# Kernel optimization log

Hardware: AMD Instinct MI355X
Metric: run time of the kernel (lower is better)

## Reference

```python
import jax, jax.numpy as jnp
import numpy as np
import math

A = 256            # n_agents == batch rows (epymarl stacks agents along batch)
B = A
OBS = 512          # obs_shape = (input_shape - n_actions) // 2
NA = 64            # n_actions
MSG = 2048         # messages_shape (divisible by A)
H = 1024           # hidden_dim
T = 3              # trajectory_length
TAU = OBS + NA
VD = MSG // A      # per-agent message dim


def setup_inputs() -> dict:
    key = jax.random.key(0)
    keys = iter(jax.random.split(key, 40))
    def lin(o, i):
        w = jax.random.normal(next(keys), (o, i), jnp.float32) * (i ** -0.5)
        return w, jnp.zeros((o,), jnp.float32)
    d = {}
    d["inputs"] = jax.random.normal(next(keys), (B, 2 * OBS + NA + MSG), jnp.float32)
    d["hidden_state"] = jax.random.normal(next(keys), (B, 3 * H), jnp.float32) * 0.1
    for name, o, i in [("pi_fc1", H, OBS + MSG), ("pi_fc2", NA, H),
                       ("fa_fc1", H, OBS), ("fa_fc2", (A - 1) * NA, H),
                       ("fo_fc1", H, NA * A + OBS), ("fo_fc2", OBS, H),
                       ("am_qs", H, MSG), ("am_ks", H, TAU), ("am_vs", VD, TAU)]:
        d[name + "_w"], d[name + "_b"] = lin(o, i)
    for name in ["pi_rnn", "fa_rnn", "fo_rnn"]:
        d[name + "_wih"], d[name + "_bih"] = lin(3 * H, H)
        d[name + "_whh"], d[name + "_bhh"] = lin(3 * H, H)
    return d


def _gru(x, h, wih, whh, bih, bhh):
    gi = x @ wih.T + bih
    gh = h @ whh.T + bhh
    ir, iz, i_n = jnp.split(gi, 3, -1)
    hr, hz, h_n = jnp.split(gh, 3, -1)
    r = jax.nn.sigmoid(ir + hr)
    z = jax.nn.sigmoid(iz + hz)
    n = jnp.tanh(i_n + r * h_n)
    return (1.0 - z) * n + z * h


def reference(inputs, hidden_state,
              pi_fc1_w, pi_fc1_b, pi_fc2_w, pi_fc2_b,
              pi_rnn_wih, pi_rnn_whh, pi_rnn_bih, pi_rnn_bhh,
              fa_fc1_w, fa_fc1_b, fa_fc2_w, fa_fc2_b,
              fa_rnn_wih, fa_rnn_whh, fa_rnn_bih, fa_rnn_bhh,
              fo_fc1_w, fo_fc1_b, fo_fc2_w, fo_fc2_b,
              fo_rnn_wih, fo_rnn_whh, fo_rnn_bih, fo_rnn_bhh,
              am_qs_w, am_qs_b, am_ks_w, am_ks_b, am_vs_w, am_vs_b):
    sg = jax.lax.stop_gradient
    lin = lambda x, w, b: x @ w.T + b
    h_fa = hidden_state[:, :H]
    h_fo = hidden_state[:, H:2 * H]
    h_pi0 = hidden_state[:, -H:]
    obs = inputs[:, :OBS]
    prev_obs = inputs[:, OBS:2 * OBS]
    prev_act = sg(inputs[:, 2 * OBS:2 * OBS + NA])   # .detach() in torch
    prev_msg = inputs[:, -MSG:]

    def pi(o, m, h):
        x = jax.nn.relu(lin(jnp.concatenate([o, m], -1), pi_fc1_w, pi_fc1_b))
        h2 = _gru(x, h, pi_rnn_wih, pi_rnn_whh, pi_rnn_bih, pi_rnn_bhh)
        return lin(h2, pi_fc2_w, pi_fc2_b), h2

    # ---- ImaginedTrajectory rollout (fixed small T, python loop is structural) ----
    o, a, h_pi = prev_obs, prev_act, h_pi0
    observations, actions = [o], [a]
    for _ in range(T - 1):
        x = jax.nn.relu(lin(o, fa_fc1_w, fa_fc1_b))
        h_fa = _gru(x, h_fa, fa_rnn_wih, fa_rnn_whh, fa_rnn_bih, fa_rnn_bhh)
        q = lin(h_fa, fa_fc2_w, fa_fc2_b)                       # [B,(A-1)*NA]
        qs = jax.nn.softmax(q.reshape(B, A - 1, NA), -1)
        # torch stack(qs_out).reshape(orig): scrambles (A-1,B) order, kept faithfully
        fa = jnp.transpose(qs, (1, 0, 2)).reshape(B, (A - 1) * NA)
        x2 = jax.nn.relu(lin(jnp.concatenate([fa, a, o], -1), fo_fc1_w, fo_fc1_b))
        h_fo = _gru(x2, h_fo, fo_rnn_wih, fo_rnn_whh, fo_rnn_bih, fo_rnn_bhh)
        nxt_o = lin(h_fo, fo_fc2_w, fo_fc2_b)
        nxt_a, h_pi = pi(sg(o), sg(prev_msg), sg(h_pi))         # forward_pi detaches inputs
        o, a = nxt_o, nxt_a
        observations.append(o)
        actions.append(a)
    taus = jnp.stack([jnp.concatenate([observations[t], actions[t]], -1)
                      for t in range(T)])                        # [T,B,TAU]

    # ---- AttentionMechanism: batched equivalent of the per-agent python loops ----
    # k rows are indexed j*n_agents + i with batch == n_agents, i.e. k[t, b] here.
    qv = lin(prev_msg, am_qs_w, am_qs_b)                         # [B,H]
    kk = jnp.einsum('tbi,hi->tbh', taus, am_ks_w) + am_ks_b      # [T,B,H]
    vv = jnp.einsum('tbi,vi->tbv', taus, am_vs_w) + am_vs_b      # [T,B,VD]
    alpha = jax.nn.softmax(jnp.einsum('bh,tbh->bt', qv, kk) / math.sqrt(H), -1)
    new_message = jnp.einsum('bt,tbv->bv', alpha, vv)            # [B,VD]

    # cat([msg]*A, 0).reshape(B,-1): each agent receives all agents' messages
    pi_msg = jnp.tile(new_message, (A, 1)).reshape(B, -1)        # [B,MSG]
    action, h_pi_f = pi(obs, pi_msg, h_pi0)                      # uses ORIGINAL h_pi slice
    h_out = jnp.concatenate([h_fa, h_fo, h_pi_f], -1)            # [B,3H]
    q_out = jnp.concatenate([new_message, action], -1)           # [B,VD+NA]
    return q_out, h_out
```

## Files before the change

### kernel.cpp

```cpp
#include <hip/hip_runtime.h>
#include <hip/hip_bf16.h>
#include <math.h>

#define OBS 512
#define MSG 2048
#define TAU 576
#define TAUP 640
#define QN 16320
#define X2W 16896
#define INW 3136
#define PIW 2560

typedef short short8v __attribute__((ext_vector_type(8)));
typedef float f32x4 __attribute__((ext_vector_type(4)));

__device__ inline unsigned bfbits(float x) {
  __hip_bfloat16 h = __float2bfloat16(x);
  return (unsigned)*reinterpret_cast<unsigned short*>(&h);
}

__device__ inline void gload16(const void* g, void* l) {
  __builtin_amdgcn_global_load_lds((__attribute__((address_space(1))) void*)(g),
                                   (__attribute__((address_space(3))) void*)(l), 16, 0, 0);
}

struct MMSet {
  const __hip_bfloat16* A;
  const __hip_bfloat16* W;
  const float* bias;
  float* C;
  __hip_bfloat16* Cb;
  int lda, ldw, ldc, ldcb;
};

template<int ACT, bool ATOMIC, bool DUAL>
__global__ __launch_bounds__(512)
void k_mm(MMSet s0, MMSet s1, int Nlim, int kSteps)
{
  __shared__ __hip_bfloat16 As[2][256 * 64];
  __shared__ __hip_bfloat16 Bs[2][64 * 64];
  const MMSet S = (DUAL && blockIdx.z) ? s1 : s0;
  const int tid = threadIdx.x;
  const int lane = tid & 63;
  const int wid = tid >> 6;
  const int m0 = blockIdx.y * 256;
  const int n0 = blockIdx.x * 64;
  const size_t k0 = ATOMIC ? (size_t)blockIdx.z * kSteps * 64 : 0;

  const __hip_bfloat16* Ab = S.A + (size_t)m0 * S.lda + k0;
  const __hip_bfloat16* Bb = S.W + (size_t)n0 * S.ldw + k0;

  int arow[4], acol[4], adst[4];
#pragma unroll
  for (int r = 0; r < 4; ++r) {
    int chunk = r * 512 + tid;
    arow[r] = chunk >> 3;
    acol[r] = ((chunk & 7) ^ (arow[r] & 7)) * 8;
    adst[r] = chunk * 8;
  }
  const int brow = tid >> 3;
  const int bcol = ((tid & 7) ^ (brow & 7)) * 8;
  const int bdst = tid * 8;

  const int wr = wid >> 1, wc = wid & 1;
  const int fr = lane & 15, q = lane >> 4;
  const int xm = fr & 7;

  f32x4 acc[4][2] = {};

  auto stage = [&](int buf, int kt) {
#pragma unroll
    for (int r = 0; r < 4; ++r)
      gload16(Ab + (size_t)arow[r] * S.lda + kt + acol[r], &As[buf][adst[r]]);
    gload16(Bb + (size_t)brow * S.ldw + kt + bcol, &Bs[buf][bdst]);
  };

  stage(0, 0);
  __syncthreads();

  for (int t = 0; t < kSteps; ++t) {
    if (t + 1 < kSteps) stage((t + 1) & 1, (t + 1) * 64);
    const __hip_bfloat16* Ac = As[t & 1];
    const __hip_bfloat16* Bc = Bs[t & 1];
#pragma unroll
    for (int ks = 0; ks < 2; ++ks) {
      const int cc = ks * 4 + q;
      const int co = ((cc ^ xm) << 3);
      short8v a0 = *(const short8v*)&Ac[(wr * 64 +  0 + fr) * 64 + co];
      short8v a1 = *(const short8v*)&Ac[(wr * 64 + 16 + fr) * 64 + co];
      short8v a2 = *(const short8v*)&Ac[(wr * 64 + 32 + fr) * 64 + co];
      short8v a3 = *(const short8v*)&Ac[(wr * 64 + 48 + fr) * 64 + co];
      short8v b0 = *(const short8v*)&Bc[(wc * 32 +  0 + fr) * 64 + co];
      short8v b1 = *(const short8v*)&Bc[(wc * 32 + 16 + fr) * 64 + co];
      acc[0][0] = __builtin_amdgcn_mfma_f32_16x16x32_bf16(a0, b0, acc[0][0], 0, 0, 0);
      acc[0][1] = __builtin_amdgcn_mfma_f32_16x16x32_bf16(a0, b1, acc[0][1], 0, 0, 0);
      acc[1][0] = __builtin_amdgcn_mfma_f32_16x16x32_bf16(a1, b0, acc[1][0], 0, 0, 0);
      acc[1][1] = __builtin_amdgcn_mfma_f32_16x16x32_bf16(a1, b1, acc[1][1], 0, 0, 0);
      acc[2][0] = __builtin_amdgcn_mfma_f32_16x16x32_bf16(a2, b0, acc[2][0], 0, 0, 0);
      acc[2][1] = __builtin_amdgcn_mfma_f32_16x16x32_bf16(a2, b1, acc[2][1], 0, 0, 0);
      acc[3][0] = __builtin_amdgcn_mfma_f32_16x16x32_bf16(a3, b0, acc[3][0], 0, 0, 0);
      acc[3][1] = __builtin_amdgcn_mfma_f32_16x16x32_bf16(a3, b1, acc[3][1], 0, 0, 0);
    }
    __syncthreads();
  }

#pragma unroll
  for (int i = 0; i < 4; ++i) {
    const int mb = m0 + wr * 64 + i * 16 + q * 4;
#pragma unroll
    for (int j = 0; j < 2; ++j) {
      const int n = n0 + wc * 32 + j * 16 + fr;
      if (n >= Nlim) continue;
      if (ATOMIC) {
#pragma unroll
        for (int v = 0; v < 4; ++v)
          atomicAdd(&S.C[(size_t)(mb + v) * S.ldc + n], acc[i][j][v]);
      } else {
        const float bb = S.bias[n];
#pragma unroll
        for (int v = 0; v < 4; ++v) {
          float val = acc[i][j][v] + bb;
          if (ACT) val = fmaxf(val, 0.f);
          if (S.C)  S.C[(size_t)(mb + v) * S.ldc + n] = val;
          if (S.Cb) S.Cb[(size_t)(mb + v) * S.ldcb + n] = __float2bfloat16(val);
        }
      }
    }
  }
}

struct CvtTable {
  const float* src[15];
  __hip_bfloat16* dst[15];
  long nchunk[15];
  int srcld[15], N[15], Kdst[15], Kval[15];
  int cumBlk[16];
};

__global__ __launch_bounds__(256)
void k_cvt_all(CvtTable T)
{
  const int bx = blockIdx.x;
  int sg = 0;
#pragma unroll
  for (int i = 1; i < 15; ++i) sg += (bx >= T.cumBlk[i]) ? 1 : 0;
  const float* src = T.src[0]; __hip_bfloat16* dst = T.dst[0];
  long nchunk = T.nchunk[0];
  int srcld = T.srcld[0], N = T.N[0], Kd = T.Kdst[0], Kv = T.Kval[0], b0 = T.cumBlk[0];
#pragma unroll
  for (int i = 1; i < 15; ++i)
    if (sg == i) { src = T.src[i]; dst = T.dst[i]; nchunk = T.nchunk[i];
                   srcld = T.srcld[i]; N = T.N[i]; Kd = T.Kdst[i]; Kv = T.Kval[i]; b0 = T.cumBlk[i]; }
  long chunk = (long)(bx - b0) * 256 + threadIdx.x;
  if (chunk >= nchunk) return;
  long idx = chunk * 8;
  int n = (int)(idx / Kd);
  int k = (int)(idx % Kd);
  uint4 o;
  if (n < N && k < Kv) {
    const float* s = src + (size_t)n * srcld + k;
    float4 v0 = *(const float4*)s;
    float4 v1 = *(const float4*)(s + 4);
    o.x = bfbits(v0.x) | (bfbits(v0.y) << 16);
    o.y = bfbits(v0.z) | (bfbits(v0.w) << 16);
    o.z = bfbits(v1.x) | (bfbits(v1.y) << 16);
    o.w = bfbits(v1.z) | (bfbits(v1.w) << 16);
  } else {
    o = make_uint4(0, 0, 0, 0);
  }
  *(uint4*)(dst + idx) = o;
}

__global__ __launch_bounds__(256)
void k_gru(const float* __restrict__ gi, const float* __restrict__ gh,
           const float* __restrict__ hs, int ldsrc,
           float* __restrict__ hd, int lddst, __hip_bfloat16* __restrict__ hb)
{
  int idx = blockIdx.x * 256 + threadIdx.x;
  int b = idx >> 10, j = idx & 1023;
  float ir = gi[b * 3072 + j];
  float iz = gi[b * 3072 + 1024 + j];
  float in_ = gi[b * 3072 + 2048 + j];
  float hr = gh[b * 3072 + j];
  float hz = gh[b * 3072 + 1024 + j];
  float hn = gh[b * 3072 + 2048 + j];
  float r = 1.f / (1.f + expf(-(ir + hr)));
  float z = 1.f / (1.f + expf(-(iz + hz)));
  float n = tanhf(in_ + r * hn);
  float h = hs[(size_t)b * ldsrc + j];
  float o = (1.f - z) * n + z * h;
  hd[(size_t)b * lddst + j] = o;
  hb[idx] = __float2bfloat16(o);
}

__global__ __launch_bounds__(256)
void k_softmax_scatter(const __hip_bfloat16* __restrict__ q, __hip_bfloat16* __restrict__ x2)
{
  int wid = blockIdx.x * 4 + (threadIdx.x >> 6);
  int lane = threadIdx.x & 63;
  int b = wid / 255, p = wid % 255;
  float v = __bfloat162float(q[(size_t)b * QN + p * 64 + lane]);
  float m = v;
#pragma unroll
  for (int s = 32; s; s >>= 1) m = fmaxf(m, __shfl_xor(m, s));
  float e = expf(v - m);
  float sum = e;
#pragma unroll
  for (int s = 32; s; s >>= 1) sum += __shfl_xor(sum, s);
  float r = e / sum;
  int flat = p * 16384 + b * 64 + lane;
  int bp = flat / QN;
  int j = flat - bp * QN;
  x2[(size_t)bp * X2W + j] = __float2bfloat16(r);
}

__global__ __launch_bounds__(256)
void k_x2_tail(const __hip_bfloat16* __restrict__ taus_t, __hip_bfloat16* __restrict__ x2)
{
  int idx = blockIdx.x * 256 + threadIdx.x;
  int b = idx / TAU, c = idx % TAU;
  if (c < 64)
    x2[(size_t)b * X2W + QN + c] = taus_t[(size_t)b * TAUP + OBS + c];
  else
    x2[(size_t)b * X2W + QN + 64 + (c - 64)] = taus_t[(size_t)b * TAUP + (c - 64)];
}

__global__ __launch_bounds__(256)
void k_concat_pi_loop(const __hip_bfloat16* __restrict__ taus_t,
                      const __hip_bfloat16* __restrict__ msg,
                      __hip_bfloat16* __restrict__ piin)
{
  int idx = blockIdx.x * 256 + threadIdx.x;
  int b = idx / PIW, c = idx % PIW;
  piin[idx] = (c < OBS) ? taus_t[(size_t)b * TAUP + c] : msg[b * MSG + (c - OBS)];
}

__global__ __launch_bounds__(256)
void k_concat_pi_final(const float* __restrict__ in, const float* __restrict__ nm,
                       __hip_bfloat16* __restrict__ piin)
{
  int idx = blockIdx.x * 256 + threadIdx.x;
  int b = idx / PIW, c = idx % PIW;
  float v = (c < OBS) ? in[(size_t)b * INW + c] : nm[c - OBS];
  piin[idx] = __float2bfloat16(v);
}

__global__ __launch_bounds__(256)
void k_init_h(const float* __restrict__ hid,
              float* __restrict__ h32a, float* __restrict__ h32o, float* __restrict__ h32p,
              __hip_bfloat16* __restrict__ hba, __hip_bfloat16* __restrict__ hbo,
              __hip_bfloat16* __restrict__ hbp, __hip_bfloat16* __restrict__ hbp0)
{
  int idx = blockIdx.x * 256 + threadIdx.x;
  int b = idx / 3072, c = idx % 3072;
  float v = hid[idx];
  __hip_bfloat16 hb = __float2bfloat16(v);
  int j = c & 1023;
  if (c < 1024)      { h32a[b * 1024 + j] = v; hba[b * 1024 + j] = hb; }
  else if (c < 2048) { h32o[b * 1024 + j] = v; hbo[b * 1024 + j] = hb; }
  else               { h32p[b * 1024 + j] = v; hbp[b * 1024 + j] = hb; hbp0[b * 1024 + j] = hb; }
}

__global__ __launch_bounds__(256)
void k_init_taus(const float* __restrict__ in, __hip_bfloat16* __restrict__ taus)
{
  int idx = blockIdx.x * 256 + threadIdx.x;
  int t = idx / (256 * TAUP);
  int r = (idx / TAUP) % 256;
  int c = idx % TAUP;
  float v = 0.f;
  if (t == 0 && c < TAU)
    v = (c < OBS) ? in[(size_t)r * INW + OBS + c]
                  : in[(size_t)r * INW + 2 * OBS + (c - OBS)];
  taus[idx] = __float2bfloat16(v);
}

__global__ __launch_bounds__(256)
void k_fill_bias(float* __restrict__ C, const float* __restrict__ bias)
{
  int idx = blockIdx.x * 256 + threadIdx.x;
  C[idx] = bias[idx & 1023];
}

__global__ __launch_bounds__(256)
void k_relu_cvt(const float* __restrict__ s, __hip_bfloat16* __restrict__ d)
{
  int idx = blockIdx.x * 256 + threadIdx.x;
  d[idx] = __float2bfloat16(fmaxf(s[idx], 0.f));
}

__global__ __launch_bounds__(64)
void k_vv(const __hip_bfloat16* __restrict__ taus, const float* __restrict__ w,
          const float* __restrict__ bias, float* __restrict__ vv)
{
  int row = blockIdx.x;
  int lane = threadIdx.x;
  const __hip_bfloat16* tr = taus + (size_t)row * TAUP;
  for (int v = 0; v < 8; ++v) {
    float s = 0.f;
    for (int k = lane; k < TAU; k += 64) s += __bfloat162float(tr[k]) * w[v * TAU + k];
#pragma unroll
    for (int d = 32; d; d >>= 1) s += __shfl_xor(s, d);
    if (lane == 0) vv[row * 8 + v] = s + bias[v];
  }
}

__global__ __launch_bounds__(64)
void k_attn(const float* __restrict__ qv, const float* __restrict__ kk,
            const float* __restrict__ vv, float* __restrict__ nm,
            float* __restrict__ out_q)
{
  int b = blockIdx.x;
  int lane = threadIdx.x;
  const float* qb = qv + (size_t)b * 1024;
  float s[3];
#pragma unroll
  for (int t = 0; t < 3; ++t) {
    const float* kb = kk + (size_t)(t * 256 + b) * 1024;
    float acc = 0.f;
    for (int h = lane; h < 1024; h += 64) acc += qb[h] * kb[h];
#pragma unroll
    for (int d = 32; d; d >>= 1) acc += __shfl_xor(acc, d);
    s[t] = acc * (1.f / 32.f);
  }
  float m = fmaxf(s[0], fmaxf(s[1], s[2]));
  float e0 = expf(s[0] - m), e1 = expf(s[1] - m), e2 = expf(s[2] - m);
  float inv = 1.f / (e0 + e1 + e2);
  float a0 = e0 * inv, a1 = e1 * inv, a2 = e2 * inv;
  if (lane < 8) {
    float v = a0 * vv[(0 * 256 + b) * 8 + lane]
            + a1 * vv[(1 * 256 + b) * 8 + lane]
            + a2 * vv[(2 * 256 + b) * 8 + lane];
    nm[b * 8 + lane] = v;
    out_q[b * 72 + lane] = v;
  }
}

__global__ __launch_bounds__(256)
void k_copy_hout(const float* __restrict__ hfa, const float* __restrict__ hfo,
                 float* __restrict__ hout)
{
  int idx = blockIdx.x * 256 + threadIdx.x;
  int b = idx / 2048, c = idx % 2048;
  float v = (c < 1024) ? hfa[b * 1024 + c] : hfo[b * 1024 + (c - 1024)];
  hout[(size_t)b * 3072 + c] = v;
}

extern "C" void kernel_launch(void* const* d_in, const int* in_sizes, int n_in,
                              void* d_out_v, int out_size, void* d_ws, size_t ws_size,
                              hipStream_t stream)
{
  const float* inputs   = (const float*)d_in[0];
  const float* hidden   = (const float*)d_in[1];
  const float* pi_fc1_w = (const float*)d_in[2];
  const float* pi_fc1_b = (const float*)d_in[3];
  const float* pi_fc2_w = (const float*)d_in[4];
  const float* pi_fc2_b = (const float*)d_in[5];
  const float* fa_fc1_w = (const float*)d_in[6];
  const float* fa_fc1_b = (const float*)d_in[7];
  const float* fa_fc2_w = (const float*)d_in[8];
  const float* fa_fc2_b = (const float*)d_in[9];
  const float* fo_fc1_w = (const float*)d_in[10];
  const float* fo_fc1_b = (const float*)d_in[11];
  const float* fo_fc2_w = (const float*)d_in[12];
  const float* fo_fc2_b = (const float*)d_in[13];
  const float* am_qs_w  = (const float*)d_in[14];
  const float* am_qs_b  = (const float*)d_in[15];
  const float* am_ks_w  = (const float*)d_in[16];
  const float* am_ks_b  = (const float*)d_in[17];
  const float* am_vs_w  = (const float*)d_in[18];
  const float* am_vs_b  = (const float*)d_in[19];
  const float* pi_wih   = (const float*)d_in[20];
  const float* pi_bih   = (const float*)d_in[21];
  const float* pi_whh   = (const float*)d_in[22];
  const float* pi_bhh   = (const float*)d_in[23];
  const float* fa_wih   = (const float*)d_in[24];
  const float* fa_bih   = (const float*)d_in[25];
  const float* fa_whh   = (const float*)d_in[26];
  const float* fa_bhh   = (const float*)d_in[27];
  const float* fo_wih   = (const float*)d_in[28];
  const float* fo_bih   = (const float*)d_in[29];
  const float* fo_whh   = (const float*)d_in[30];
  const float* fo_bhh   = (const float*)d_in[31];

  float* out = (float*)d_out_v;
  char* p = (char*)d_ws;
  auto alloc = [&](size_t bytes) { void* r = p; p += (bytes + 255) & ~(size_t)255; return r; };
  typedef __hip_bfloat16 bf;

  bf* WPI1 = (bf*)alloc((size_t)1024 * 2560 * 2);
  bf* WPI2 = (bf*)alloc((size_t)64 * 1024 * 2);
  bf* WFA1 = (bf*)alloc((size_t)1024 * 512 * 2);
  bf* WFA2 = (bf*)alloc((size_t)16384 * 1024 * 2);
  bf* WFO1 = (bf*)alloc((size_t)1024 * 16896 * 2);
  bf* WFO2 = (bf*)alloc((size_t)512 * 1024 * 2);
  bf* WQS  = (bf*)alloc((size_t)1024 * 2048 * 2);
  bf* WKS  = (bf*)alloc((size_t)1024 * TAUP * 2);
  bf* WPIIH = (bf*)alloc((size_t)3072 * 1024 * 2);
  bf* WPIHH = (bf*)alloc((size_t)3072 * 1024 * 2);
  bf* WFAIH = (bf*)alloc((size_t)3072 * 1024 * 2);
  bf* WFAHH = (bf*)alloc((size_t)3072 * 1024 * 2);
  bf* WFOIH = (bf*)alloc((size_t)3072 * 1024 * 2);
  bf* WFOHH = (bf*)alloc((size_t)3072 * 1024 * 2);
  bf* HFAB = (bf*)alloc((size_t)256 * 1024 * 2);
  bf* HFOB = (bf*)alloc((size_t)256 * 1024 * 2);
  bf* HPIB = (bf*)alloc((size_t)256 * 1024 * 2);
  bf* HPI0B = (bf*)alloc((size_t)256 * 1024 * 2);
  bf* XBUFB = (bf*)alloc((size_t)256 * 1024 * 2);
  bf* TAUSB = (bf*)alloc((size_t)3 * 256 * TAUP * 2);
  bf* X2B  = (bf*)alloc((size_t)256 * X2W * 2);
  bf* PIINB = (bf*)alloc((size_t)256 * PIW * 2);
  bf* MSGB = (bf*)alloc((size_t)256 * MSG * 2);
  bf* QBUFB = (bf*)alloc((size_t)256 * QN * 2);
  float* HFA32 = (float*)alloc((size_t)256 * 1024 * 4);
  float* HFO32 = (float*)alloc((size_t)256 * 1024 * 4);
  float* HPI32 = (float*)alloc((size_t)256 * 1024 * 4);
  float* XBUF32 = (float*)alloc((size_t)256 * 1024 * 4);
  float* GI = (float*)alloc((size_t)256 * 3072 * 4);
  float* GH = (float*)alloc((size_t)256 * 3072 * 4);
  float* QV = (float*)alloc((size_t)256 * 1024 * 4);
  float* KK = (float*)alloc((size_t)768 * 1024 * 4);
  float* VV = (float*)alloc((size_t)768 * 8 * 4);
  float* NM = (float*)alloc((size_t)2048 * 4);

  CvtTable T;
  int nseg = 0; int blk = 0;
  auto addseg = [&](const float* src, int srcld, bf* dst, int N, int Kdst, int Kval, int Npad) {
    long ch = (long)Npad * Kdst / 8;
    T.src[nseg] = src; T.dst[nseg] = dst; T.nchunk[nseg] = ch;
    T.srcld[nseg] = srcld; T.N[nseg] = N; T.Kdst[nseg] = Kdst; T.Kval[nseg] = Kval;
    T.cumBlk[nseg] = blk;
    blk += (int)((ch + 255) / 256);
    ++nseg;
  };
  addseg(pi_fc1_w, 2560, WPI1, 1024, 2560, 2560, 1024);
  addseg(pi_fc2_w, 1024, WPI2, 64, 1024, 1024, 64);
  addseg(fa_fc1_w, 512,  WFA1, 1024, 512, 512, 1024);
  addseg(fa_fc2_w, 1024, WFA2, 16320, 1024, 1024, 16384);
  addseg(fo_fc1_w, 16896, WFO1, 1024, 16896, 16896, 1024);
  addseg(fo_fc2_w, 1024, WFO2, 512, 1024, 1024, 512);
  addseg(am_qs_w, 2048, WQS, 1024, 2048, 2048, 1024);
  addseg(am_ks_w, 576, WKS, 1024, TAUP, 576, 1024);
  addseg(pi_wih, 1024, WPIIH, 3072, 1024, 1024, 3072);
  addseg(pi_whh, 1024, WPIHH, 3072, 1024, 1024, 3072);
  addseg(fa_wih, 1024, WFAIH, 3072, 1024, 1024, 3072);
  addseg(fa_whh, 1024, WFAHH, 3072, 1024, 1024, 3072);
  addseg(fo_wih, 1024, WFOIH, 3072, 1024, 1024, 3072);
  addseg(fo_whh, 1024, WFOHH, 3072, 1024, 1024, 3072);
  addseg(inputs + 1088, INW, MSGB, 256, 2048, 2048, 256);
  T.cumBlk[15] = blk;

  auto mset = [&](const bf* A, int lda, const bf* W, int ldw, const float* bias,
                  float* C, int ldc, bf* Cb, int ldcb) {
    MMSet s; s.A = A; s.W = W; s.bias = bias; s.C = C; s.Cb = Cb;
    s.lda = lda; s.ldw = ldw; s.ldc = ldc; s.ldcb = ldcb; return s;
  };
  auto mm = [&](MMSet a, int M, int Npad, int Nlim, int K, int act) {
    dim3 g(Npad / 64, M / 256, 1);
    if (act) k_mm<1, false, false><<<g, 512, 0, stream>>>(a, a, Nlim, K / 64);
    else     k_mm<0, false, false><<<g, 512, 0, stream>>>(a, a, Nlim, K / 64);
  };
  auto mmDual = [&](MMSet a, MMSet b, int Npad, int K) {
    dim3 g(Npad / 64, 1, 2);
    k_mm<0, false, true><<<g, 512, 0, stream>>>(a, b, Npad, K / 64);
  };

  k_cvt_all<<<blk, 256, 0, stream>>>(T);
  k_init_h<<<3072, 256, 0, stream>>>(hidden, HFA32, HFO32, HPI32, HFAB, HFOB, HPIB, HPI0B);
  k_init_taus<<<3 * TAUP, 256, 0, stream>>>(inputs, TAUSB);

  for (int t = 0; t < 2; ++t) {
    bf* taus_t = TAUSB + (size_t)t * 256 * TAUP;
    bf* taus_n = TAUSB + (size_t)(t + 1) * 256 * TAUP;
    mm(mset(taus_t, TAUP, WFA1, 512, fa_fc1_b, nullptr, 0, XBUFB, 1024), 256, 1024, 1024, 512, 1);
    mmDual(mset(XBUFB, 1024, WFAIH, 1024, fa_bih, GI, 3072, nullptr, 0),
           mset(HFAB, 1024, WFAHH, 1024, fa_bhh, GH, 3072, nullptr, 0), 3072, 1024);
    k_gru<<<1024, 256, 0, stream>>>(GI, GH, HFA32, 1024, HFA32, 1024, HFAB);
    mm(mset(HFAB, 1024, WFA2, 1024, fa_fc2_b, nullptr, 0, QBUFB, QN), 256, 16384, QN, 1024, 0);
    k_x2_tail<<<576, 256, 0, stream>>>(taus_t, X2B);
    k_softmax_scatter<<<16320, 256, 0, stream>>>(QBUFB, X2B);
    k_fill_bias<<<1024, 256, 0, stream>>>(XBUF32, fo_fc1_b);
    {
      dim3 g(16, 1, 12);
      MMSet s = mset(X2B, X2W, WFO1, X2W, fo_fc1_b, XBUF32, 1024, nullptr, 0);
      k_mm<0, true, false><<<g, 512, 0, stream>>>(s, s, 1024, 22);
    }
    k_relu_cvt<<<1024, 256, 0, stream>>>(XBUF32, XBUFB);
    mmDual(mset(XBUFB, 1024, WFOIH, 1024, fo_bih, GI, 3072, nullptr, 0),
           mset(HFOB, 1024, WFOHH, 1024, fo_bhh, GH, 3072, nullptr, 0), 3072, 1024);
    k_gru<<<1024, 256, 0, stream>>>(GI, GH, HFO32, 1024, HFO32, 1024, HFOB);
    mm(mset(HFOB, 1024, WFO2, 1024, fo_fc2_b, nullptr, 0, taus_n, TAUP), 256, 512, 512, 1024, 0);
    k_concat_pi_loop<<<2560, 256, 0, stream>>>(taus_t, MSGB, PIINB);
    mm(mset(PIINB, PIW, WPI1, PIW, pi_fc1_b, nullptr, 0, XBUFB, 1024), 256, 1024, 1024, PIW, 1);
    mmDual(mset(XBUFB, 1024, WPIIH, 1024, pi_bih, GI, 3072, nullptr, 0),
           mset(HPIB, 1024, WPIHH, 1024, pi_bhh, GH, 3072, nullptr, 0), 3072, 1024);
    k_gru<<<1024, 256, 0, stream>>>(GI, GH, HPI32, 1024, HPI32, 1024, HPIB);
    mm(mset(HPIB, 1024, WPI2, 1024, pi_fc2_b, nullptr, 0, taus_n + OBS, TAUP), 256, 64, 64, 1024, 0);
  }

  mm(mset(MSGB, MSG, WQS, MSG, am_qs_b, QV, 1024, nullptr, 0), 256, 1024, 1024, 2048, 0);
  mm(mset(TAUSB, TAUP, WKS, TAUP, am_ks_b, KK, 1024, nullptr, 0), 768, 1024, 1024, TAUP, 0);
  k_vv<<<768, 64, 0, stream>>>(TAUSB, am_vs_w, am_vs_b, VV);
  k_attn<<<256, 64, 0, stream>>>(QV, KK, VV, NM, out);

  k_concat_pi_final<<<2560, 256, 0, stream>>>(inputs, NM, PIINB);
  mm(mset(PIINB, PIW, WPI1, PIW, pi_fc1_b, nullptr, 0, XBUFB, 1024), 256, 1024, 1024, PIW, 1);
  mmDual(mset(XBUFB, 1024, WPIIH, 1024, pi_bih, GI, 3072, nullptr, 0),
         mset(HPI0B, 1024, WPIHH, 1024, pi_bhh, GH, 3072, nullptr, 0), 3072, 1024);
  k_gru<<<1024, 256, 0, stream>>>(GI, GH, hidden + 2048, 3072,
                                  out + 256 * 72 + 2048, 3072, HPIB);
  mm(mset(HPIB, 1024, WPI2, 1024, pi_fc2_b, out + 8, 72, nullptr, 0), 256, 64, 64, 1024, 0);
  k_copy_hout<<<2048, 256, 0, stream>>>(HFA32, HFO32, out + 256 * 72);
  (void)in_sizes; (void)n_in; (void)out_size; (void)ws_size;
}
```

Baseline: 736.8 us.

## Read fp32 weights directly in GEMM and drop the upfront bf16 conversion pass

The separate kernel that converted every fp32 weight matrix to padded bf16 copies in workspace is removed. The GEMM now loads fp32 weight tiles into registers, converts them to bf16 and writes them to LDS, while the activation tiles still use async global-to-LDS loads. The M tile size becomes a template parameter (64/128/256) so the small-M GEMMs launch more blocks. The hidden-state, taus and message init kernels are merged into one launch. The change avoids the full read-and-write of the weights in a conversion pass, but it doubles the bytes read for weights inside each GEMM and adds register conversion work to the main loop.

```diff
diff --git a/kernel.cpp b/kernel.cpp
--- a/kernel.cpp
+++ b/kernel.cpp
@@ -14,9 +14,9 @@
 typedef short short8v __attribute__((ext_vector_type(8)));
 typedef float f32x4 __attribute__((ext_vector_type(4)));
 
-__device__ inline unsigned bfbits(float x) {
+__device__ inline unsigned short bfbits(float x) {
   __hip_bfloat16 h = __float2bfloat16(x);
-  return (unsigned)*reinterpret_cast<unsigned short*>(&h);
+  return *reinterpret_cast<unsigned short*>(&h);
 }
 
 __device__ inline void gload16(const void* g, void* l) {
@@ -26,91 +26,109 @@
 
 struct MMSet {
   const __hip_bfloat16* A;
-  const __hip_bfloat16* W;
+  const float* W;
   const float* bias;
   float* C;
   __hip_bfloat16* Cb;
   int lda, ldw, ldc, ldcb;
 };
 
-template<int ACT, bool ATOMIC, bool DUAL>
+template<int BM, int ACT, bool ATOMIC, bool DUAL>
 __global__ __launch_bounds__(512)
-void k_mm(MMSet s0, MMSet s1, int Nlim, int kSteps)
-{
-  __shared__ __hip_bfloat16 As[2][256 * 64];
+void k_mm(MMSet s0, MMSet s1, int kSteps)
+{
+  constexpr int AREP = BM / 64;
+  __shared__ __hip_bfloat16 As[2][BM * 64];
   __shared__ __hip_bfloat16 Bs[2][64 * 64];
   const MMSet S = (DUAL && blockIdx.z) ? s1 : s0;
   const int tid = threadIdx.x;
   const int lane = tid & 63;
   const int wid = tid >> 6;
-  const int m0 = blockIdx.y * 256;
+  const int m0 = blockIdx.y * BM;
   const int n0 = blockIdx.x * 64;
   const size_t k0 = ATOMIC ? (size_t)blockIdx.z * kSteps * 64 : 0;
 
   const __hip_bfloat16* Ab = S.A + (size_t)m0 * S.lda + k0;
-  const __hip_bfloat16* Bb = S.W + (size_t)n0 * S.ldw + k0;
-
-  int arow[4], acol[4], adst[4];
-#pragma unroll
-  for (int r = 0; r < 4; ++r) {
+  const float* Bb = S.W + (size_t)n0 * S.ldw + k0;
+
+  int arow[AREP], acol[AREP], adst[AREP];
+#pragma unroll
+  for (int r = 0; r < AREP; ++r) {
     int chunk = r * 512 + tid;
     arow[r] = chunk >> 3;
     acol[r] = ((chunk & 7) ^ (arow[r] & 7)) * 8;
     adst[r] = chunk * 8;
   }
-  const int brow = tid >> 3;
-  const int bcol = ((tid & 7) ^ (brow & 7)) * 8;
-  const int bdst = tid * 8;
+  int brow[2], bcol[2], bdst[2];
+#pragma unroll
+  for (int r = 0; r < 2; ++r) {
+    int c = r * 512 + tid;
+    brow[r] = c >> 4;
+    int g = (c & 15) >> 1, half = c & 1;
+    bcol[r] = (c & 15) * 4;
+    bdst[r] = brow[r] * 64 + ((g ^ (brow[r] & 7)) << 3) + half * 4;
+  }
 
   const int wr = wid >> 1, wc = wid & 1;
   const int fr = lane & 15, q = lane >> 4;
   const int xm = fr & 7;
 
-  f32x4 acc[4][2] = {};
-
-  auto stage = [&](int buf, int kt) {
-#pragma unroll
-    for (int r = 0; r < 4; ++r)
+  f32x4 acc[AREP][2] = {};
+  float4 bv0, bv1;
+
+  auto stageA = [&](int buf, int kt) {
+#pragma unroll
+    for (int r = 0; r < AREP; ++r)
       gload16(Ab + (size_t)arow[r] * S.lda + kt + acol[r], &As[buf][adst[r]]);
-    gload16(Bb + (size_t)brow * S.ldw + kt + bcol, &Bs[buf][bdst]);
-  };
-
-  stage(0, 0);
+  };
+  auto loadB = [&](int kt) {
+    bv0 = *(const float4*)(Bb + (size_t)brow[0] * S.ldw + kt + bcol[0]);
+    bv1 = *(const float4*)(Bb + (size_t)brow[1] * S.ldw + kt + bcol[1]);
+  };
+  auto writeB = [&](int buf) {
+    ushort4 w0, w1;
+    w0.x = bfbits(bv0.x); w0.y = bfbits(bv0.y); w0.z = bfbits(bv0.z); w0.w = bfbits(bv0.w);
+    w1.x = bfbits(bv1.x); w1.y = bfbits(bv1.y); w1.z = bfbits(bv1.z); w1.w = bfbits(bv1.w);
+    *(ushort4*)&Bs[buf][bdst[0]] = w0;
+    *(ushort4*)&Bs[buf][bdst[1]] = w1;
+  };
+
+  stageA(0, 0);
+  loadB(0);
+  writeB(0);
   __syncthreads();
 
   for (int t = 0; t < kSteps; ++t) {
-    if (t + 1 < kSteps) stage((t + 1) & 1, (t + 1) * 64);
-    const __hip_bfloat16* Ac = As[t & 1];
-    const __hip_bfloat16* Bc = Bs[t & 1];
+    const int buf = t & 1;
+    if (t + 1 < kSteps) {
+      stageA(buf ^ 1, (t + 1) * 64);
+      loadB((t + 1) * 64);
+    }
+    const __hip_bfloat16* Ac = As[buf];
+    const __hip_bfloat16* Bc = Bs[buf];
 #pragma unroll
     for (int ks = 0; ks < 2; ++ks) {
       const int cc = ks * 4 + q;
       const int co = ((cc ^ xm) << 3);
-      short8v a0 = *(const short8v*)&Ac[(wr * 64 +  0 + fr) * 64 + co];
-      short8v a1 = *(const short8v*)&Ac[(wr * 64 + 16 + fr) * 64 + co];
-      short8v a2 = *(const short8v*)&Ac[(wr * 64 + 32 + fr) * 64 + co];
-      short8v a3 = *(const short8v*)&Ac[(wr * 64 + 48 + fr) * 64 + co];
       short8v b0 = *(const short8v*)&Bc[(wc * 32 +  0 + fr) * 64 + co];
       short8v b1 = *(const short8v*)&Bc[(wc * 32 + 16 + fr) * 64 + co];
-      acc[0][0] = __builtin_amdgcn_mfma_f32_16x16x32_bf16(a0, b0, acc[0][0], 0, 0, 0);
-      acc[0][1] = __builtin_amdgcn_mfma_f32_16x16x32_bf16(a0, b1, acc[0][1], 0, 0, 0);
-      acc[1][0] = __builtin_amdgcn_mfma_f32_16x16x32_bf16(a1, b0, acc[1][0], 0, 0, 0);
-      acc[1][1] = __builtin_amdgcn_mfma_f32_16x16x32_bf16(a1, b1, acc[1][1], 0, 0, 0);
-      acc[2][0] = __builtin_amdgcn_mfma_f32_16x16x32_bf16(a2, b0, acc[2][0], 0, 0, 0);
-      acc[2][1] = __builtin_amdgcn_mfma_f32_16x16x32_bf16(a2, b1, acc[2][1], 0, 0, 0);
-      acc[3][0] = __builtin_amdgcn_mfma_f32_16x16x32_bf16(a3, b0, acc[3][0], 0, 0, 0);
-      acc[3][1] = __builtin_amdgcn_mfma_f32_16x16x32_bf16(a3, b1, acc[3][1], 0, 0, 0);
+#pragma unroll
+      for (int i = 0; i < AREP; ++i) {
+        short8v a = *(const short8v*)&Ac[(wr * (AREP * 16) + i * 16 + fr) * 64 + co];
+        acc[i][0] = __builtin_amdgcn_mfma_f32_16x16x32_bf16(a, b0, acc[i][0], 0, 0, 0);
+        acc[i][1] = __builtin_amdgcn_mfma_f32_16x16x32_bf16(a, b1, acc[i][1], 0, 0, 0);
+      }
     }
+    if (t + 1 < kSteps) writeB(buf ^ 1);
     __syncthreads();
   }
 
 #pragma unroll
-  for (int i = 0; i < 4; ++i) {
-    const int mb = m0 + wr * 64 + i * 16 + q * 4;
+  for (int i = 0; i < AREP; ++i) {
+    const int mb = m0 + wr * (AREP * 16) + i * 16 + q * 4;
 #pragma unroll
     for (int j = 0; j < 2; ++j) {
       const int n = n0 + wc * 32 + j * 16 + fr;
-      if (n >= Nlim) continue;
       if (ATOMIC) {
 #pragma unroll
         for (int v = 0; v < 4; ++v)
@@ -129,46 +147,38 @@
   }
 }
 
-struct CvtTable {
-  const float* src[15];
-  __hip_bfloat16* dst[15];
-  long nchunk[15];
-  int srcld[15], N[15], Kdst[15], Kval[15];
-  int cumBlk[16];
-};
-
-__global__ __launch_bounds__(256)
-void k_cvt_all(CvtTable T)
+__global__ __launch_bounds__(256)
+void k_init(const float* __restrict__ in, const float* __restrict__ hid,
+            float* __restrict__ h32a, float* __restrict__ h32o, float* __restrict__ h32p,
+            __hip_bfloat16* __restrict__ hba, __hip_bfloat16* __restrict__ hbo,
+            __hip_bfloat16* __restrict__ hbp, __hip_bfloat16* __restrict__ hbp0,
+            __hip_bfloat16* __restrict__ taus, __hip_bfloat16* __restrict__ msgb)
 {
   const int bx = blockIdx.x;
-  int sg = 0;
-#pragma unroll
-  for (int i = 1; i < 15; ++i) sg += (bx >= T.cumBlk[i]) ? 1 : 0;
-  const float* src = T.src[0]; __hip_bfloat16* dst = T.dst[0];
-  long nchunk = T.nchunk[0];
-  int srcld = T.srcld[0], N = T.N[0], Kd = T.Kdst[0], Kv = T.Kval[0], b0 = T.cumBlk[0];
-#pragma unroll
-  for (int i = 1; i < 15; ++i)
-    if (sg == i) { src = T.src[i]; dst = T.dst[i]; nchunk = T.nchunk[i];
-                   srcld = T.srcld[i]; N = T.N[i]; Kd = T.Kdst[i]; Kv = T.Kval[i]; b0 = T.cumBlk[i]; }
-  long chunk = (long)(bx - b0) * 256 + threadIdx.x;
-  if (chunk >= nchunk) return;
-  long idx = chunk * 8;
-  int n = (int)(idx / Kd);
-  int k = (int)(idx % Kd);
-  uint4 o;
-  if (n < N && k < Kv) {
-    const float* s = src + (size_t)n * srcld + k;
-    float4 v0 = *(const float4*)s;
-    float4 v1 = *(const float4*)(s + 4);
-    o.x = bfbits(v0.x) | (bfbits(v0.y) << 16);
-    o.y = bfbits(v0.z) | (bfbits(v0.w) << 16);
-    o.z = bfbits(v1.x) | (bfbits(v1.y) << 16);
-    o.w = bfbits(v1.z) | (bfbits(v1.w) << 16);
+  if (bx < 3072) {
+    int idx = bx * 256 + threadIdx.x;
+    int b = idx / 3072, c = idx % 3072;
+    float v = hid[idx];
+    __hip_bfloat16 hb = __float2bfloat16(v);
+    int j = c & 1023;
+    if (c < 1024)      { h32a[b * 1024 + j] = v; hba[b * 1024 + j] = hb; }
+    else if (c < 2048) { h32o[b * 1024 + j] = v; hbo[b * 1024 + j] = hb; }
+    else               { h32p[b * 1024 + j] = v; hbp[b * 1024 + j] = hb; hbp0[b * 1024 + j] = hb; }
+  } else if (bx < 3072 + 1920) {
+    int idx = (bx - 3072) * 256 + threadIdx.x;
+    int t = idx / (256 * TAUP);
+    int r = (idx / TAUP) % 256;
+    int c = idx % TAUP;
+    float v = 0.f;
+    if (t == 0 && c < TAU)
+      v = (c < OBS) ? in[(size_t)r * INW + OBS + c]
+                    : in[(size_t)r * INW + 2 * OBS + (c - OBS)];
+    taus[idx] = __float2bfloat16(v);
   } else {
-    o = make_uint4(0, 0, 0, 0);
-  }
-  *(uint4*)(dst + idx) = o;
+    int idx = (bx - 3072 - 1920) * 256 + threadIdx.x;
+    int b = idx >> 11, c = idx & 2047;
+    msgb[idx] = __float2bfloat16(in[(size_t)b * INW + 1088 + c]);
+  }
 }
 
 __global__ __launch_bounds__(256)
@@ -243,36 +253,6 @@
   int b = idx / PIW, c = idx % PIW;
   float v = (c < OBS) ? in[(size_t)b * INW + c] : nm[c - OBS];
   piin[idx] = __float2bfloat16(v);
-}
-
-__global__ __launch_bounds__(256)
-void k_init_h(const float* __restrict__ hid,
-              float* __restrict__ h32a, float* __restrict__ h32o, float* __restrict__ h32p,
-              __hip_bfloat16* __restrict__ hba, __hip_bfloat16* __restrict__ hbo,
-              __hip_bfloat16* __restrict__ hbp, __hip_bfloat16* __restrict__ hbp0)
-{
-  int idx = blockIdx.x * 256 + threadIdx.x;
-  int b = idx / 3072, c = idx % 3072;
-  float v = hid[idx];
-  __hip_bfloat16 hb = __float2bfloat16(v);
-  int j = c & 1023;
-  if (c < 1024)      { h32a[b * 1024 + j] = v; hba[b * 1024 + j] = hb; }
-  else if (c < 2048) { h32o[b * 1024 + j] = v; hbo[b * 1024 + j] = hb; }
-  else               { h32p[b * 1024 + j] = v; hbp[b * 1024 + j] = hb; hbp0[b * 1024 + j] = hb; }
-}
-
-__global__ __launch_bounds__(256)
-void k_init_taus(const float* __restrict__ in, __hip_bfloat16* __restrict__ taus)
-{
-  int idx = blockIdx.x * 256 + threadIdx.x;
-  int t = idx / (256 * TAUP);
-  int r = (idx / TAUP) % 256;
-  int c = idx % TAUP;
-  float v = 0.f;
-  if (t == 0 && c < TAU)
-    v = (c < OBS) ? in[(size_t)r * INW + OBS + c]
-                  : in[(size_t)r * INW + 2 * OBS + (c - OBS)];
-  taus[idx] = __float2bfloat16(v);
 }
 
 __global__ __launch_bounds__(256)
@@ -388,20 +368,6 @@
   auto alloc = [&](size_t bytes) { void* r = p; p += (bytes + 255) & ~(size_t)255; return r; };
   typedef __hip_bfloat16 bf;
 
-  bf* WPI1 = (bf*)alloc((size_t)1024 * 2560 * 2);
-  bf* WPI2 = (bf*)alloc((size_t)64 * 1024 * 2);
-  bf* WFA1 = (bf*)alloc((size_t)1024 * 512 * 2);
-  bf* WFA2 = (bf*)alloc((size_t)16384 * 1024 * 2);
-  bf* WFO1 = (bf*)alloc((size_t)1024 * 16896 * 2);
-  bf* WFO2 = (bf*)alloc((size_t)512 * 1024 * 2);
-  bf* WQS  = (bf*)alloc((size_t)1024 * 2048 * 2);
-  bf* WKS  = (bf*)alloc((size_t)1024 * TAUP * 2);
-  bf* WPIIH = (bf*)alloc((size_t)3072 * 1024 * 2);
-  bf* WPIHH = (bf*)alloc((size_t)3072 * 1024 * 2);
-  bf* WFAIH = (bf*)alloc((size_t)3072 * 1024 * 2);
-  bf* WFAHH = (bf*)alloc((size_t)3072 * 1024 * 2);
-  bf* WFOIH = (bf*)alloc((size_t)3072 * 1024 * 2);
-  bf* WFOHH = (bf*)alloc((size_t)3072 * 1024 * 2);
   bf* HFAB = (bf*)alloc((size_t)256 * 1024 * 2);
   bf* HFOB = (bf*)alloc((size_t)256 * 1024 * 2);
   bf* HPIB = (bf*)alloc((size_t)256 * 1024 * 2);
@@ -423,93 +389,73 @@
   float* VV = (float*)alloc((size_t)768 * 8 * 4);
   float* NM = (float*)alloc((size_t)2048 * 4);
 
-  CvtTable T;
-  int nseg = 0; int blk = 0;
-  auto addseg = [&](const float* src, int srcld, bf* dst, int N, int Kdst, int Kval, int Npad) {
-    long ch = (long)Npad * Kdst / 8;
-    T.src[nseg] = src; T.dst[nseg] = dst; T.nchunk[nseg] = ch;
-    T.srcld[nseg] = srcld; T.N[nseg] = N; T.Kdst[nseg] = Kdst; T.Kval[nseg] = Kval;
-    T.cumBlk[nseg] = blk;
-    blk += (int)((ch + 255) / 256);
-    ++nseg;
-  };
-  addseg(pi_fc1_w, 2560, WPI1, 1024, 2560, 2560, 1024);
-  addseg(pi_fc2_w, 1024, WPI2, 64, 1024, 1024, 64);
-  addseg(fa_fc1_w, 512,  WFA1, 1024, 512, 512, 1024);
-  addseg(fa_fc2_w, 1024, WFA2, 16320, 1024, 1024, 16384);
-  addseg(fo_fc1_w, 16896, WFO1, 1024, 16896, 16896, 1024);
-  addseg(fo_fc2_w, 1024, WFO2, 512, 1024, 1024, 512);
-  addseg(am_qs_w, 2048, WQS, 1024, 2048, 2048, 1024);
-  addseg(am_ks_w, 576, WKS, 1024, TAUP, 576, 1024);
-  addseg(pi_wih, 1024, WPIIH, 3072, 1024, 1024, 3072);
-  addseg(pi_whh, 1024, WPIHH, 3072, 1024, 1024, 3072);
-  addseg(fa_wih, 1024, WFAIH, 3072, 1024, 1024, 3072);
-  addseg(fa_whh, 1024, WFAHH, 3072, 1024, 1024, 3072);
-  addseg(fo_wih, 1024, WFOIH, 3072, 1024, 1024, 3072);
-  addseg(fo_whh, 1024, WFOHH, 3072, 1024, 1024, 3072);
-  addseg(inputs + 1088, INW, MSGB, 256, 2048, 2048, 256);
-  T.cumBlk[15] = blk;
-
-  auto mset = [&](const bf* A, int lda, const bf* W, int ldw, const float* bias,
+  auto mset = [&](const bf* A, int lda, const float* W, int ldw, const float* bias,
                   float* C, int ldc, bf* Cb, int ldcb) {
     MMSet s; s.A = A; s.W = W; s.bias = bias; s.C = C; s.Cb = Cb;
     s.lda = lda; s.ldw = ldw; s.ldc = ldc; s.ldcb = ldcb; return s;
   };
-  auto mm = [&](MMSet a, int M, int Npad, int Nlim, int K, int act) {
-    dim3 g(Npad / 64, M / 256, 1);
-    if (act) k_mm<1, false, false><<<g, 512, 0, stream>>>(a, a, Nlim, K / 64);
-    else     k_mm<0, false, false><<<g, 512, 0, stream>>>(a, a, Nlim, K / 64);
-  };
-  auto mmDual = [&](MMSet a, MMSet b, int Npad, int K) {
-    dim3 g(Npad / 64, 1, 2);
-    k_mm<0, false, true><<<g, 512, 0, stream>>>(a, b, Npad, K / 64);
-  };
-
-  k_cvt_all<<<blk, 256, 0, stream>>>(T);
-  k_init_h<<<3072, 256, 0, stream>>>(hidden, HFA32, HFO32, HPI32, HFAB, HFOB, HPIB, HPI0B);
-  k_init_taus<<<3 * TAUP, 256, 0, stream>>>(inputs, TAUSB);
+  auto mm256 = [&](MMSet a, int M, int N, int K) {
+    dim3 g(N / 64, M / 256, 1);
+    k_mm<256, 0, false, false><<<g, 512, 0, stream>>>(a, a, K / 64);
+  };
+  auto mm128 = [&](MMSet a, int M, int N, int K) {
+    dim3 g(N / 64, M / 128, 1);
+    k_mm<128, 0, false, false><<<g, 512, 0, stream>>>(a, a, K / 64);
+  };
+  auto mm64 = [&](MMSet a, int N, int K, int act) {
+    dim3 g(N / 64, 4, 1);
+    if (act) k_mm<64, 1, false, false><<<g, 512, 0, stream>>>(a, a, K / 64);
+    else     k_mm<64, 0, false, false><<<g, 512, 0, stream>>>(a, a, K / 64);
+  };
+  auto mmDual = [&](MMSet a, MMSet b, int N, int K) {
+    dim3 g(N / 64, 2, 2);
+    k_mm<128, 0, false, true><<<g, 512, 0, stream>>>(a, b, K / 64);
+  };
+
+  k_init<<<3072 + 1920 + 2048, 256, 0, stream>>>(inputs, hidden,
+      HFA32, HFO32, HPI32, HFAB, HFOB, HPIB, HPI0B, TAUSB, MSGB);
 
   for (int t = 0; t < 2; ++t) {
     bf* taus_t = TAUSB + (size_t)t * 256 * TAUP;
     bf* taus_n = TAUSB + (size_t)(t + 1) * 256 * TAUP;
-    mm(mset(taus_t, TAUP, WFA1, 512, fa_fc1_b, nullptr, 0, XBUFB, 1024), 256, 1024, 1024, 512, 1);
-    mmDual(mset(XBUFB, 1024, WFAIH, 1024, fa_bih, GI, 3072, nullptr, 0),
-           mset(HFAB, 1024, WFAHH, 1024, fa_bhh, GH, 3072, nullptr, 0), 3072, 1024);
+    mm64(mset(taus_t, TAUP, fa_fc1_w, 512, fa_fc1_b, nullptr, 0, XBUFB, 1024), 1024, 512, 1);
+    mmDual(mset(XBUFB, 1024, fa_wih, 1024, fa_bih, GI, 3072, nullptr, 0),
+           mset(HFAB, 1024, fa_whh, 1024, fa_bhh, GH, 3072, nullptr, 0), 3072, 1024);
     k_gru<<<1024, 256, 0, stream>>>(GI, GH, HFA32, 1024, HFA32, 1024, HFAB);
-    mm(mset(HFAB, 1024, WFA2, 1024, fa_fc2_b, nullptr, 0, QBUFB, QN), 256, 16384, QN, 1024, 0);
+    mm256(mset(HFAB, 1024, fa_fc2_w, 1024, fa_fc2_b, nullptr, 0, QBUFB, QN), 256, QN, 1024);
     k_x2_tail<<<576, 256, 0, stream>>>(taus_t, X2B);
     k_softmax_scatter<<<16320, 256, 0, stream>>>(QBUFB, X2B);
     k_fill_bias<<<1024, 256, 0, stream>>>(XBUF32, fo_fc1_b);
     {
       dim3 g(16, 1, 12);
-      MMSet s = mset(X2B, X2W, WFO1, X2W, fo_fc1_b, XBUF32, 1024, nullptr, 0);
-      k_mm<0, true, false><<<g, 512, 0, stream>>>(s, s, 1024, 22);
+      MMSet s = mset(X2B, X2W, fo_fc1_w, X2W, fo_fc1_b, XBUF32, 1024, nullptr, 0);
+      k_mm<256, 0, true, false><<<g, 512, 0, stream>>>(s, s, 22);
     }
     k_relu_cvt<<<1024, 256, 0, stream>>>(XBUF32, XBUFB);
-    mmDual(mset(XBUFB, 1024, WFOIH, 1024, fo_bih, GI, 3072, nullptr, 0),
-           mset(HFOB, 1024, WFOHH, 1024, fo_bhh, GH, 3072, nullptr, 0), 3072, 1024);
+    mmDual(mset(XBUFB, 1024, fo_wih, 1024, fo_bih, GI, 3072, nullptr, 0),
+           mset(HFOB, 1024, fo_whh, 1024, fo_bhh, GH, 3072, nullptr, 0), 3072, 1024);
     k_gru<<<1024, 256, 0, stream>>>(GI, GH, HFO32, 1024, HFO32, 1024, HFOB);
-    mm(mset(HFOB, 1024, WFO2, 1024, fo_fc2_b, nullptr, 0, taus_n, TAUP), 256, 512, 512, 1024, 0);
+    mm64(mset(HFOB, 1024, fo_fc2_w, 1024, fo_fc2_b, nullptr, 0, taus_n, TAUP), 512, 1024, 0);
     k_concat_pi_loop<<<2560, 256, 0, stream>>>(taus_t, MSGB, PIINB);
-    mm(mset(PIINB, PIW, WPI1, PIW, pi_fc1_b, nullptr, 0, XBUFB, 1024), 256, 1024, 1024, PIW, 1);
-    mmDual(mset(XBUFB, 1024, WPIIH, 1024, pi_bih, GI, 3072, nullptr, 0),
-           mset(HPIB, 1024, WPIHH, 1024, pi_bhh, GH, 3072, nullptr, 0), 3072, 1024);
+    mm64(mset(PIINB, PIW, pi_fc1_w, PIW, pi_fc1_b, nullptr, 0, XBUFB, 1024), 1024, PIW, 1);
+    mmDual(mset(XBUFB, 1024, pi_wih, 1024, pi_bih, GI, 3072, nullptr, 0),
+           mset(HPIB, 1024, pi_whh, 1024, pi_bhh, GH, 3072, nullptr, 0), 3072, 1024);
     k_gru<<<1024, 256, 0, stream>>>(GI, GH, HPI32, 1024, HPI32, 1024, HPIB);
-    mm(mset(HPIB, 1024, WPI2, 1024, pi_fc2_b, nullptr, 0, taus_n + OBS, TAUP), 256, 64, 64, 1024, 0);
-  }
-
-  mm(mset(MSGB, MSG, WQS, MSG, am_qs_b, QV, 1024, nullptr, 0), 256, 1024, 1024, 2048, 0);
-  mm(mset(TAUSB, TAUP, WKS, TAUP, am_ks_b, KK, 1024, nullptr, 0), 768, 1024, 1024, TAUP, 0);
+    mm64(mset(HPIB, 1024, pi_fc2_w, 1024, pi_fc2_b, nullptr, 0, taus_n + OBS, TAUP), 64, 1024, 0);
+  }
+
+  mm64(mset(MSGB, MSG, am_qs_w, MSG, am_qs_b, QV, 1024, nullptr, 0), 1024, 2048, 0);
+  mm128(mset(TAUSB, TAUP, am_ks_w, TAU, am_ks_b, KK, 1024, nullptr, 0), 768, 1024, TAU);
   k_vv<<<768, 64, 0, stream>>>(TAUSB, am_vs_w, am_vs_b, VV);
   k_attn<<<256, 64, 0, stream>>>(QV, KK, VV, NM, out);
 
   k_concat_pi_final<<<2560, 256, 0, stream>>>(inputs, NM, PIINB);
-  mm(mset(PIINB, PIW, WPI1, PIW, pi_fc1_b, nullptr, 0, XBUFB, 1024), 256, 1024, 1024, PIW, 1);
-  mmDual(mset(XBUFB, 1024, WPIIH, 1024, pi_bih, GI, 3072, nullptr, 0),
-         mset(HPI0B, 1024, WPIHH, 1024, pi_bhh, GH, 3072, nullptr, 0), 3072, 1024);
+  mm64(mset(PIINB, PIW, pi_fc1_w, PIW, pi_fc1_b, nullptr, 0, XBUFB, 1024), 1024, PIW, 1);
+  mmDual(mset(XBUFB, 1024, pi_wih, 1024, pi_bih, GI, 3072, nullptr, 0),
+         mset(HPI0B, 1024, pi_whh, 1024, pi_bhh, GH, 3072, nullptr, 0), 3072, 1024);
   k_gru<<<1024, 256, 0, stream>>>(GI, GH, hidden + 2048, 3072,
                                   out + 256 * 72 + 2048, 3072, HPIB);
-  mm(mset(HPIB, 1024, WPI2, 1024, pi_fc2_b, out + 8, 72, nullptr, 0), 256, 64, 64, 1024, 0);
+  mm64(mset(HPIB, 1024, pi_fc2_w, 1024, pi_fc2_b, out + 8, 72, nullptr, 0), 64, 1024, 0);
   k_copy_hout<<<2048, 256, 0, stream>>>(HFA32, HFO32, out + 256 * 72);
   (void)in_sizes; (void)n_in; (void)out_size; (void)ws_size;
 }
```

After: 611.9 us. -17.0%, faster.
